# Optimization experiments

Hardware: AMD Instinct MI355X
Metric: run time of the kernel (lower is better)

## Reference

```python
import jax, jax.numpy as jnp
import numpy as np

K = 7          # kernel_size
PAD = 3        # padding (same-size output)
GROUPS = 8


def _unfold(z, H, W):
    # z: [B, C, H+2p, W+2p] -> patches [B, C, H, W, K*K], flat index = kh*K + kw
    # matches torch .unfold(2,K,1).unfold(3,K,1).view(..., -1)
    return jnp.stack(
        [z[:, :, a:a + H, b:b + W] for a in range(K) for b in range(K)],
        axis=-1,
    )


def setup_inputs() -> dict:
    key = jax.random.key(0)
    ks = jax.random.split(key, 7)
    B, C, H, W = 4, 64, 64, 64
    Cout = 64
    fan_scale = (2.0 / Cout) ** 0.5  # kaiming fan_out, 1x1 conv
    return {
        "x": jax.random.normal(ks[0], (B, C, H, W), jnp.float32),
        "y": jax.random.normal(ks[1], (B, C, H, W), jnp.float32),
        "Wq": jax.random.normal(ks[2], (Cout, C), jnp.float32) * fan_scale,
        "Wk": jax.random.normal(ks[3], (Cout, C), jnp.float32) * fan_scale,
        "Wv": jax.random.normal(ks[4], (Cout, C), jnp.float32) * fan_scale,
        "rel_h": jax.random.normal(ks[5], (Cout // 2, K), jnp.float32),
        "rel_w": jax.random.normal(ks[6], (Cout // 2, K), jnp.float32),
    }


def reference(x, y, Wq, Wk, Wv, rel_h, rel_w):
    B, C, H, W = x.shape
    Cout = Wq.shape[0]
    half = Cout // 2

    # 1x1 convs (no bias) commute with zero padding, so project first.
    q = jnp.einsum('oc,bchw->bohw', Wq, x)          # [B, Cout, H, W]
    k_full = jnp.einsum('oc,bchw->bohw', Wk, x)
    v_full = jnp.einsum('oc,bchw->bohw', Wv, y)

    pad4 = ((0, 0), (0, 0), (PAD, PAD), (PAD, PAD))
    k_pat = _unfold(jnp.pad(k_full, pad4), H, W)    # [B, Cout, H, W, K*K]
    v_pat = _unfold(jnp.pad(v_full, pad4), H, W)

    # relative-position bias: rel_h over kh (top half of channels), rel_w over kw
    bias_h = jnp.broadcast_to(rel_h[:, :, None], (half, K, K))   # [Cout/2, kh, kw]
    bias_w = jnp.broadcast_to(rel_w[:, None, :], (half, K, K))
    bias = jnp.concatenate([bias_h, bias_w], axis=0).reshape(Cout, K * K)
    k_pat = k_pat + bias[None, :, None, None, :]

    cg = Cout // GROUPS
    k_pat = k_pat.reshape(B, GROUPS, cg, H, W, K * K)
    v_pat = v_pat.reshape(B, GROUPS, cg, H, W, K * K)
    q = q.reshape(B, GROUPS, cg, H, W, 1)

    attn = jax.nn.softmax(q * k_pat, axis=-1)       # per-channel softmax over window
    out = jnp.sum(attn * v_pat, axis=-1)            # [B, G, cg, H, W]
    return out.reshape(B, Cout, H, W)
```

## Files before the change

kernel.cpp:

```cpp
#include <hip/hip_runtime.h>

#define HW    4096
#define C_IN  64
#define C_OUT 64

typedef float f4 __attribute__((ext_vector_type(4)));

__global__ __launch_bounds__(256) void proj_kernel(
    const float* __restrict__ x, const float* __restrict__ y,
    const float* __restrict__ Wq, const float* __restrict__ Wk,
    const float* __restrict__ Wv,
    float* __restrict__ q, float* __restrict__ k, float* __restrict__ v)
{
    const int px  = blockIdx.x * 256 + threadIdx.x;
    const int b   = px >> 12;
    const int pib = px & 4095;
    const int g   = blockIdx.y;

    const float* xb = x + (size_t)b * C_IN * HW + pib;
    const float* yb = y + (size_t)b * C_IN * HW + pib;

    float accq[8], acck[8], accv[8];
#pragma unroll
    for (int i = 0; i < 8; ++i) { accq[i] = 0.f; acck[i] = 0.f; accv[i] = 0.f; }

#pragma unroll 4
    for (int c = 0; c < C_IN; ++c) {
        const float xv = xb[(size_t)c * HW];
        const float yv = yb[(size_t)c * HW];
#pragma unroll
        for (int i = 0; i < 8; ++i) {
            const int co = g * 8 + i;
            accq[i] = fmaf(Wq[co * C_IN + c], xv, accq[i]);
            acck[i] = fmaf(Wk[co * C_IN + c], xv, acck[i]);
            accv[i] = fmaf(Wv[co * C_IN + c], yv, accv[i]);
        }
    }

#pragma unroll
    for (int i = 0; i < 8; ++i) {
        const int co = g * 8 + i;
        const size_t o = ((size_t)b * C_OUT + co) * HW + pib;
        q[o] = accq[i];
        k[o] = acck[i];
        v[o] = accv[i];
    }
}

__global__ __launch_bounds__(256) void attn_kernel(
    const float* __restrict__ q, const float* __restrict__ k,
    const float* __restrict__ v,
    const float* __restrict__ rel_h, const float* __restrict__ rel_w,
    float* __restrict__ out)
{
    const int blk = blockIdx.x;
    const int bc  = blk >> 2;
    const int h0  = (blk & 3) * 16;
    const int c   = bc & 63;
    const int t   = threadIdx.x;
    const int r   = t >> 4;
    const int cgp = t & 15;
    const int h   = h0 + r;
    const int w0  = cgp * 4;

    const float* kimg = k + (size_t)bc * HW;
    const float* vimg = v + (size_t)bc * HW;

    const f4 qv = *(const f4*)(q + (size_t)bc * HW + h * 64 + w0);
    float l[4] = {0.f, 0.f, 0.f, 0.f};
    float o[4] = {0.f, 0.f, 0.f, 0.f};

    const bool lok = (cgp > 0);
    const bool rko = (cgp < 15);

#pragma unroll
    for (int a = 0; a < 7; ++a) {
        const int  hy = h + a - 3;
        const bool rv = ((unsigned)hy < 64u);
        const float* krow = kimg + hy * 64 + w0;
        const float* vrow = vimg + hy * 64 + w0;
        const f4 z = {0.f, 0.f, 0.f, 0.f};

        const f4 k0 = (rv && lok) ? *(const f4*)(krow - 4) : z;
        const f4 k1 =  rv         ? *(const f4*)(krow)     : z;
        const f4 k2 = (rv && rko) ? *(const f4*)(krow + 4) : z;
        const f4 v0 = (rv && lok) ? *(const f4*)(vrow - 4) : z;
        const f4 v1 =  rv         ? *(const f4*)(vrow)     : z;
        const f4 v2 = (rv && rko) ? *(const f4*)(vrow + 4) : z;

        const float kw[12] = {k0[0], k0[1], k0[2], k0[3],
                              k1[0], k1[1], k1[2], k1[3],
                              k2[0], k2[1], k2[2], k2[3]};
        const float vw[12] = {v0[0], v0[1], v0[2], v0[3],
                              v1[0], v1[1], v1[2], v1[3],
                              v2[0], v2[1], v2[2], v2[3]};

        const float bh = rel_h[(c & 31) * 7 + a];

#pragma unroll
        for (int b2 = 0; b2 < 7; ++b2) {
            const float bias = (c < 32) ? bh : rel_w[(c - 32) * 7 + b2];
#pragma unroll
            for (int p = 0; p < 4; ++p) {
                float s = qv[p] * (kw[p + b2 + 1] + bias);
                s = fminf(s, 80.f);
                const float e = __expf(s);
                l[p] += e;
                o[p] = fmaf(e, vw[p + b2 + 1], o[p]);
            }
        }
    }

    f4 res;
#pragma unroll
    for (int p = 0; p < 4; ++p)
        res[p] = o[p] * __builtin_amdgcn_rcpf(l[p]);
    *(f4*)(out + (size_t)bc * HW + h * 64 + w0) = res;
}

extern "C" void kernel_launch(void* const* d_in, const int* in_sizes, int n_in,
                              void* d_out, int out_size, void* d_ws, size_t ws_size,
                              hipStream_t stream) {
    const float* x   = (const float*)d_in[0];
    const float* y   = (const float*)d_in[1];
    const float* Wq  = (const float*)d_in[2];
    const float* Wk  = (const float*)d_in[3];
    const float* Wv  = (const float*)d_in[4];
    const float* rlh = (const float*)d_in[5];
    const float* rlw = (const float*)d_in[6];
    float* out = (float*)d_out;

    float* q = (float*)d_ws;
    float* k = q + (1 << 20);
    float* v = k + (1 << 20);

    dim3 gA(16384 / 256, 8);
    proj_kernel<<<gA, 256, 0, stream>>>(x, y, Wq, Wk, Wv, q, k, v);
    attn_kernel<<<1024, 256, 0, stream>>>(q, k, v, rlh, rlw, out);
}
```

Measured before the change: 114.9 us.

## Stage K/V halo tiles and projection weights in LDS, fold bias into exp2

The projection kernel now stages its 8-output-channel weight slices for Wq/Wk/Wv in shared memory and reads them as float4 vectors, replacing scalar global weight loads. The attention kernel loads a zero-padded 22x72 K and V halo tile into LDS once per block, which removes the per-thread bounds checks and redundant global loads. The softmax is rewritten to exp2 with q pre-scaled by log2e and q*bias precomputed, so each score becomes a single fma. The bias branch is specialised by template. This adds LDS usage and barriers, and changes the clamp threshold to match the base-2 domain.

New measurement: 109.9 us. -4.4%, faster.

```diff
diff --git a/kernel.cpp b/kernel.cpp
--- a/kernel.cpp
+++ b/kernel.cpp
@@ -1,8 +1,6 @@
 #include <hip/hip_runtime.h>
 
-#define HW    4096
-#define C_IN  64
-#define C_OUT 64
+#define HW 4096
 
 typedef float f4 __attribute__((ext_vector_type(4)));
 
@@ -12,110 +10,167 @@
     const float* __restrict__ Wv,
     float* __restrict__ q, float* __restrict__ k, float* __restrict__ v)
 {
-    const int px  = blockIdx.x * 256 + threadIdx.x;
+    __shared__ float wlds[64 * 24];
+    const int t = threadIdx.x;
+    const int g = blockIdx.y;
+
+#pragma unroll
+    for (int m = 0; m < 3; ++m) {
+        const float* W = (m == 0) ? Wq : (m == 1) ? Wk : Wv;
+#pragma unroll
+        for (int hh = 0; hh < 2; ++hh) {
+            const int r = hh * 256 + t;
+            const int i = r >> 6, c = r & 63;
+            wlds[c * 24 + m * 8 + i] = W[g * 512 + r];
+        }
+    }
+    __syncthreads();
+
+    const int px  = blockIdx.x * 256 + t;
     const int b   = px >> 12;
     const int pib = px & 4095;
-    const int g   = blockIdx.y;
+    const float* xb = x + (size_t)b * 64 * HW + pib;
+    const float* yb = y + (size_t)b * 64 * HW + pib;
 
-    const float* xb = x + (size_t)b * C_IN * HW + pib;
-    const float* yb = y + (size_t)b * C_IN * HW + pib;
+    float aq[8], ak[8], av[8];
+#pragma unroll
+    for (int i = 0; i < 8; ++i) { aq[i] = 0.f; ak[i] = 0.f; av[i] = 0.f; }
 
-    float accq[8], acck[8], accv[8];
+#pragma unroll 16
+    for (int c = 0; c < 64; ++c) {
+        const float xv = xb[c * HW];
+        const float yv = yb[c * HW];
+        const f4 wq0 = *(const f4*)&wlds[c * 24 + 0];
+        const f4 wq1 = *(const f4*)&wlds[c * 24 + 4];
+        const f4 wk0 = *(const f4*)&wlds[c * 24 + 8];
+        const f4 wk1 = *(const f4*)&wlds[c * 24 + 12];
+        const f4 wv0 = *(const f4*)&wlds[c * 24 + 16];
+        const f4 wv1 = *(const f4*)&wlds[c * 24 + 20];
 #pragma unroll
-    for (int i = 0; i < 8; ++i) { accq[i] = 0.f; acck[i] = 0.f; accv[i] = 0.f; }
-
-#pragma unroll 4
-    for (int c = 0; c < C_IN; ++c) {
-        const float xv = xb[(size_t)c * HW];
-        const float yv = yb[(size_t)c * HW];
-#pragma unroll
-        for (int i = 0; i < 8; ++i) {
-            const int co = g * 8 + i;
-            accq[i] = fmaf(Wq[co * C_IN + c], xv, accq[i]);
-            acck[i] = fmaf(Wk[co * C_IN + c], xv, acck[i]);
-            accv[i] = fmaf(Wv[co * C_IN + c], yv, accv[i]);
+        for (int i = 0; i < 4; ++i) {
+            aq[i]     = fmaf(wq0[i], xv, aq[i]);
+            aq[i + 4] = fmaf(wq1[i], xv, aq[i + 4]);
+            ak[i]     = fmaf(wk0[i], xv, ak[i]);
+            ak[i + 4] = fmaf(wk1[i], xv, ak[i + 4]);
+            av[i]     = fmaf(wv0[i], yv, av[i]);
+            av[i + 4] = fmaf(wv1[i], yv, av[i + 4]);
         }
     }
 
 #pragma unroll
     for (int i = 0; i < 8; ++i) {
-        const int co = g * 8 + i;
-        const size_t o = ((size_t)b * C_OUT + co) * HW + pib;
-        q[o] = accq[i];
-        k[o] = acck[i];
-        v[o] = accv[i];
+        const size_t o = ((size_t)b * 64 + g * 8 + i) * HW + pib;
+        q[o] = aq[i];
+        k[o] = ak[i];
+        v[o] = av[i];
     }
 }
 
-__global__ __launch_bounds__(256) void attn_kernel(
-    const float* __restrict__ q, const float* __restrict__ k,
-    const float* __restrict__ v,
-    const float* __restrict__ rel_h, const float* __restrict__ rel_w,
-    float* __restrict__ out)
+template<bool BIAS_H>
+__device__ __forceinline__ void attn_body(
+    const float* kT, const float* vT, int r, int w0,
+    const float qe[4], const float qb[7][4], float l[4], float o[4])
 {
-    const int blk = blockIdx.x;
-    const int bc  = blk >> 2;
-    const int h0  = (blk & 3) * 16;
-    const int c   = bc & 63;
-    const int t   = threadIdx.x;
-    const int r   = t >> 4;
-    const int cgp = t & 15;
-    const int h   = h0 + r;
-    const int w0  = cgp * 4;
-
-    const float* kimg = k + (size_t)bc * HW;
-    const float* vimg = v + (size_t)bc * HW;
-
-    const f4 qv = *(const f4*)(q + (size_t)bc * HW + h * 64 + w0);
-    float l[4] = {0.f, 0.f, 0.f, 0.f};
-    float o[4] = {0.f, 0.f, 0.f, 0.f};
-
-    const bool lok = (cgp > 0);
-    const bool rko = (cgp < 15);
-
 #pragma unroll
     for (int a = 0; a < 7; ++a) {
-        const int  hy = h + a - 3;
-        const bool rv = ((unsigned)hy < 64u);
-        const float* krow = kimg + hy * 64 + w0;
-        const float* vrow = vimg + hy * 64 + w0;
-        const f4 z = {0.f, 0.f, 0.f, 0.f};
-
-        const f4 k0 = (rv && lok) ? *(const f4*)(krow - 4) : z;
-        const f4 k1 =  rv         ? *(const f4*)(krow)     : z;
-        const f4 k2 = (rv && rko) ? *(const f4*)(krow + 4) : z;
-        const f4 v0 = (rv && lok) ? *(const f4*)(vrow - 4) : z;
-        const f4 v1 =  rv         ? *(const f4*)(vrow)     : z;
-        const f4 v2 = (rv && rko) ? *(const f4*)(vrow + 4) : z;
-
-        const float kw[12] = {k0[0], k0[1], k0[2], k0[3],
-                              k1[0], k1[1], k1[2], k1[3],
+        const float* kr = &kT[(r + a) * 72 + w0];
+        const float* vr = &vT[(r + a) * 72 + w0];
+        const f4 k0 = *(const f4*)(kr), k1 = *(const f4*)(kr + 4), k2 = *(const f4*)(kr + 8);
+        const f4 v0 = *(const f4*)(vr), v1 = *(const f4*)(vr + 4), v2 = *(const f4*)(vr + 8);
+        const float kw[12] = {k0[0], k0[1], k0[2], k0[3], k1[0], k1[1], k1[2], k1[3],
                               k2[0], k2[1], k2[2], k2[3]};
-        const float vw[12] = {v0[0], v0[1], v0[2], v0[3],
-                              v1[0], v1[1], v1[2], v1[3],
+        const float vw[12] = {v0[0], v0[1], v0[2], v0[3], v1[0], v1[1], v1[2], v1[3],
                               v2[0], v2[1], v2[2], v2[3]};
-
-        const float bh = rel_h[(c & 31) * 7 + a];
-
 #pragma unroll
         for (int b2 = 0; b2 < 7; ++b2) {
-            const float bias = (c < 32) ? bh : rel_w[(c - 32) * 7 + b2];
 #pragma unroll
             for (int p = 0; p < 4; ++p) {
-                float s = qv[p] * (kw[p + b2 + 1] + bias);
-                s = fminf(s, 80.f);
-                const float e = __expf(s);
+                float s = fmaf(qe[p], kw[p + b2 + 1], qb[BIAS_H ? a : b2][p]);
+                s = fminf(s, 115.0f);
+                const float e = __builtin_amdgcn_exp2f(s);
                 l[p] += e;
                 o[p] = fmaf(e, vw[p + b2 + 1], o[p]);
             }
         }
     }
+}
+
+__global__ __launch_bounds__(256) void attn_kernel(
+    const float* __restrict__ qg, const float* __restrict__ kg,
+    const float* __restrict__ vg,
+    const float* __restrict__ rel_h, const float* __restrict__ rel_w,
+    float* __restrict__ out)
+{
+    __shared__ float kT[22 * 72];
+    __shared__ float vT[22 * 72];
+
+    const int blk = blockIdx.x;
+    const int bc  = blk >> 2;
+    const int h0  = (blk & 3) << 4;
+    const int c   = bc & 63;
+    const int t   = threadIdx.x;
+
+    const float* kimg = kg + (size_t)bc * HW;
+    const float* vimg = vg + (size_t)bc * HW;
+    const f4 z4 = {0.f, 0.f, 0.f, 0.f};
+
+    if (t < 88) {
+        const int row = t >> 2, side = (t >> 1) & 1, arr = t & 1;
+        float* dst = arr ? vT : kT;
+        *(f4*)&dst[row * 72 + side * 68] = z4;
+    }
+#pragma unroll
+    for (int j = 0; j < 2; ++j) {
+        const int idx = j * 256 + t;
+        if (idx < 352) {
+            const int row = idx >> 4, ch = idx & 15;
+            const int hy = h0 - 3 + row;
+            const bool rv = ((unsigned)hy < 64u);
+            const f4 kv = rv ? *(const f4*)&kimg[hy * 64 + ch * 4] : z4;
+            const f4 vv = rv ? *(const f4*)&vimg[hy * 64 + ch * 4] : z4;
+            *(f4*)&kT[row * 72 + ch * 4 + 4] = kv;
+            *(f4*)&vT[row * 72 + ch * 4 + 4] = vv;
+        }
+    }
+    __syncthreads();
+
+    const int r  = t >> 4;
+    const int w0 = (t & 15) << 2;
+    const int h  = h0 + r;
+
+    const float LOG2E = 1.4426950408889634f;
+    const f4 qv = *(const f4*)&qg[(size_t)bc * HW + h * 64 + w0];
+    float qe[4];
+#pragma unroll
+    for (int p = 0; p < 4; ++p) qe[p] = qv[p] * LOG2E;
+
+    float qb[7][4];
+    if (c < 32) {
+#pragma unroll
+        for (int a = 0; a < 7; ++a) {
+            const float bh = rel_h[c * 7 + a];
+#pragma unroll
+            for (int p = 0; p < 4; ++p) qb[a][p] = qe[p] * bh;
+        }
+    } else {
+#pragma unroll
+        for (int j = 0; j < 7; ++j) {
+            const float bw = rel_w[(c - 32) * 7 + j];
+#pragma unroll
+            for (int p = 0; p < 4; ++p) qb[j][p] = qe[p] * bw;
+        }
+    }
+
+    float l[4] = {0.f, 0.f, 0.f, 0.f};
+    float o[4] = {0.f, 0.f, 0.f, 0.f};
+    if (c < 32) attn_body<true >(kT, vT, r, w0, qe, qb, l, o);
+    else        attn_body<false>(kT, vT, r, w0, qe, qb, l, o);
 
     f4 res;
 #pragma unroll
     for (int p = 0; p < 4; ++p)
         res[p] = o[p] * __builtin_amdgcn_rcpf(l[p]);
-    *(f4*)(out + (size_t)bc * HW + h * 64 + w0) = res;
+    *(f4*)&out[(size_t)bc * HW + h * 64 + w0] = res;
 }
 
 extern "C" void kernel_launch(void* const* d_in, const int* in_sizes, int n_in,
@@ -134,7 +189,7 @@
     float* k = q + (1 << 20);
     float* v = k + (1 << 20);
 
-    dim3 gA(16384 / 256, 8);
+    dim3 gA(64, 8);
     proj_kernel<<<gA, 256, 0, stream>>>(x, y, Wq, Wk, Wv, q, k, v);
     attn_kernel<<<1024, 256, 0, stream>>>(q, k, v, rlh, rlw, out);
 }
```
